# Optimization experiments

Measured on AMD Instinct MI355X. Metric: run time of the kernel, lower is better.

## Reference

```python
import jax, jax.numpy as jnp
import numpy as np

B, S, D = 2, 2048, 1024
H = 16
HD = D // H  # 64


def _rope_tables(seq_len, head_dim, dtype=jnp.float32):
    inv_freq = 1.0 / (10000.0 ** (jnp.arange(0, head_dim, 2, dtype=jnp.float32) / head_dim))
    t = jnp.arange(seq_len, dtype=jnp.float32)
    freqs = jnp.einsum('i,j->ij', t, inv_freq)            # [S, HD/2]
    emb = jnp.concatenate([freqs, freqs], axis=-1)        # [S, HD]
    return jnp.cos(emb).astype(dtype)[None, None], jnp.sin(emb).astype(dtype)[None, None]


def _rotate_half(x):
    x1, x2 = x[..., : x.shape[-1] // 2], x[..., x.shape[-1] // 2 :]
    return jnp.concatenate([-x2, x1], axis=-1)


def setup_inputs() -> dict:
    key = jax.random.key(0)
    ks = jax.random.split(key, 9)
    s = 0.02
    return {
        'hidden_states': jax.random.normal(ks[0], (B, S, D), jnp.float32),
        'attention_mask': jnp.zeros((B, 1, S, S), jnp.float32),
        'Wq': jax.random.normal(ks[1], (D, D), jnp.float32) * s,
        'bq': jnp.zeros((D,), jnp.float32),
        'Wk': jax.random.normal(ks[2], (D, D), jnp.float32) * s,
        'bk': jnp.zeros((D,), jnp.float32),
        'Wv': jax.random.normal(ks[3], (D, D), jnp.float32) * s,
        'bv': jnp.zeros((D,), jnp.float32),
        'Wo': jax.random.normal(ks[4], (D, D), jnp.float32) * s,
        'bo': jnp.zeros((D,), jnp.float32),
    }


def reference(hidden_states, attention_mask, Wq, bq, Wk, bk, Wv, bv, Wo, bo):
    b, s = hidden_states.shape[:2]
    q = hidden_states @ Wq.T + bq
    k = hidden_states @ Wk.T + bk
    v = hidden_states @ Wv.T + bv
    # [B, H, S, HD]
    q = q.reshape(b, s, H, HD).transpose(0, 2, 1, 3)
    k = k.reshape(b, s, H, HD).transpose(0, 2, 1, 3)
    v = v.reshape(b, s, H, HD).transpose(0, 2, 1, 3)
    cos, sin = _rope_tables(s, HD, q.dtype)
    q = q * cos + _rotate_half(q) * sin
    k = k * cos + _rotate_half(k) * sin
    scaling = HD ** (-0.5)
    scores = jnp.einsum('bhqd,bhkd->bhqk', q, k) * scaling
    scores = scores / jnp.log(jnp.asarray(float(s), scores.dtype))  # dynamic NTK
    scores = scores + attention_mask
    probs = jax.nn.softmax(scores, axis=-1)
    out = jnp.einsum('bhqk,bhkd->bhqd', probs, v)
    out = out.transpose(0, 2, 1, 3).reshape(b, s, H * HD)
    return out @ Wo.T + bo
```

## Files before the change

### kernel.cpp

```cpp
#include <hip/hip_runtime.h>
#include <math.h>

#define S_LEN 2048
#define NHEAD 16
#define HDIM  64

typedef __attribute__((ext_vector_type(8))) short bf16x8;
typedef __attribute__((ext_vector_type(4))) float f32x4;

__device__ __forceinline__ unsigned short f2bf(float f) {
    union { float f; unsigned u; } v; v.f = f;
    unsigned r = v.u + 0x7fffu + ((v.u >> 16) & 1u);
    return (unsigned short)(r >> 16);
}

__device__ __forceinline__ void gl2lds16(const void* g, void* l) {
    __builtin_amdgcn_global_load_lds(
        (__attribute__((address_space(1))) void*)(void*)(g),
        (__attribute__((address_space(3))) void*)(l), 16, 0, 0);
}

__global__ __launch_bounds__(256) void convert_kernel(
    const float* __restrict__ hs, const float* __restrict__ Wq,
    const float* __restrict__ Wk, const float* __restrict__ Wv,
    const float* __restrict__ Wo, unsigned short* __restrict__ dst,
    float2* __restrict__ rtab)
{
    const int bid = blockIdx.x;
    if (bid >= 8192) {
        const int gid = (bid - 8192) * 256 + threadIdx.x;
        const int s = gid >> 5, i = gid & 31;
        const float l2c = 0.41524101186092029f;
        const float freq = exp2f(-(float)i * l2c);
        const float ang = (float)s * freq;
        float2 cs;
        cs.x = cosf(ang);
        cs.y = sinf(ang);
        rtab[gid] = cs;
        return;
    }
    const int gid = bid * 256 + threadIdx.x;
    const int n = gid << 2;
    const float* src; int off;
    if (n < (4 << 20))      { src = hs; off = n; }
    else if (n < (5 << 20)) { src = Wq; off = n - (4 << 20); }
    else if (n < (6 << 20)) { src = Wk; off = n - (5 << 20); }
    else if (n < (7 << 20)) { src = Wv; off = n - (6 << 20); }
    else                    { src = Wo; off = n - (7 << 20); }
    const float4 v = *(const float4*)(src + off);
    ushort4 o;
    o.x = f2bf(v.x); o.y = f2bf(v.y); o.z = f2bf(v.z); o.w = f2bf(v.w);
    *(ushort4*)(dst + n) = o;
}

__global__ __launch_bounds__(256, 3) void qkv_gemm_kernel(
    const unsigned short* __restrict__ X,
    const unsigned short* __restrict__ Wall,
    const float* __restrict__ bq, const float* __restrict__ bk,
    const float* __restrict__ bv, const float2* __restrict__ rtab,
    unsigned short* __restrict__ qo, unsigned short* __restrict__ ko,
    unsigned short* __restrict__ vo)
{
    __shared__ unsigned short As[128 * 64];
    __shared__ unsigned short Bs[128 * 64];

    const int mat = blockIdx.x >> 3;
    const int n0  = (blockIdx.x & 7) << 7;
    const int m0  = blockIdx.y << 7;
    const unsigned short* W = Wall + (mat << 20);
    const float* bias = (mat == 0) ? bq : (mat == 1) ? bk : bv;
    unsigned short* out = (mat == 0) ? qo : (mat == 1) ? ko : vo;

    const int tid = threadIdx.x;
    const int wave = tid >> 6, lane = tid & 63;
    const int quad = lane >> 4, ln = lane & 15;
    const int wm = (wave >> 1) << 6, wn = (wave & 1) << 6;

    const unsigned short* xptr[4];
    const unsigned short* wptr[4];
    #pragma unroll
    for (int L = 0; L < 4; ++L) {
        const int i = tid + (L << 8);
        const int r = i >> 3, cl = i & 7;
        const int cg = (cl ^ (r & 7)) << 3;
        const int rq = r & 63;
        const int tau = (mat < 2)
            ? ((r & 64) | ((rq & 15) << 1) | ((rq >> 4) & 1) | (((rq >> 5) & 1) << 5))
            : ((r & 64) | ((rq & 15) << 2) | (rq >> 4));
        xptr[L] = X + (m0 + r) * 1024 + cg;
        wptr[L] = W + (n0 + tau) * 1024 + cg;
    }

    f32x4 acc[4][4] = {};

    for (int k0 = 0; k0 < 1024; k0 += 64) {
        #pragma unroll
        for (int L = 0; L < 4; ++L) {
            const int i = tid + (L << 8);
            gl2lds16(xptr[L] + k0, &As[i << 3]);
            gl2lds16(wptr[L] + k0, &Bs[i << 3]);
        }
        __syncthreads();
        #pragma unroll
        for (int s = 0; s < 2; ++s) {
            bf16x8 a[4], b[4];
            #pragma unroll
            for (int t = 0; t < 4; ++t) {
                const int ra = wm + (t << 4) + ln;
                a[t] = *(const bf16x8*)&As[(ra << 6) + ((((s << 2) | quad) ^ (ra & 7)) << 3)];
                const int rb = wn + (t << 4) + ln;
                b[t] = *(const bf16x8*)&Bs[(rb << 6) + ((((s << 2) | quad) ^ (rb & 7)) << 3)];
            }
            #pragma unroll
            for (int i = 0; i < 4; ++i)
                #pragma unroll
                for (int j = 0; j < 4; ++j)
                    acc[i][j] = __builtin_amdgcn_mfma_f32_16x16x32_bf16(a[i], b[j], acc[i][j], 0, 0, 0);
        }
        __syncthreads();
    }

    const int h = (n0 + wn) >> 6;

    if (mat < 2) {
        const int nb = n0 + wn + (ln << 1);
        const float b0 = bias[nb],      b1 = bias[nb + 1];
        const float b2 = bias[nb + 32], b3 = bias[nb + 33];
        #pragma unroll
        for (int i = 0; i < 4; ++i) {
            #pragma unroll
            for (int reg = 0; reg < 4; ++reg) {
                const int m = m0 + wm + (i << 4) + (quad << 2) + reg;
                const int b_ = m >> 11, s_ = m & 2047;
                unsigned short* o = out + ((((b_ << 4) + h) << 11) + s_) * 64;
                const float4 cs = *(const float4*)(rtab + (s_ << 5) + (ln << 1));
                const float x1a = acc[i][0][reg] + b0, x1b = acc[i][1][reg] + b1;
                const float x2a = acc[i][2][reg] + b2, x2b = acc[i][3][reg] + b3;
                const float r0a = x1a * cs.x - x2a * cs.y;
                const float r0b = x1b * cs.z - x2b * cs.w;
                const float r1a = x2a * cs.x + x1a * cs.y;
                const float r1b = x2b * cs.z + x1b * cs.w;
                const unsigned ua = __float_as_uint(r0a) + 0x8000u;
                const unsigned ub = __float_as_uint(r0b) + 0x8000u;
                const unsigned uc = __float_as_uint(r1a) + 0x8000u;
                const unsigned ud = __float_as_uint(r1b) + 0x8000u;
                *(unsigned*)(o + (ln << 1))      = __builtin_amdgcn_perm(ub, ua, 0x07060302u);
                *(unsigned*)(o + 32 + (ln << 1)) = __builtin_amdgcn_perm(ud, uc, 0x07060302u);
            }
        }
    } else {
        const float4 bv4 = *(const float4*)(bias + n0 + wn + (ln << 2));
        #pragma unroll
        for (int i = 0; i < 4; ++i)
            #pragma unroll
            for (int reg = 0; reg < 4; ++reg) {
                const int m = m0 + wm + (i << 4) + (quad << 2) + reg;
                const int b_ = m >> 11, s_ = m & 2047;
                unsigned short* o = out + ((((b_ << 4) + h) << 11) + s_) * 64;
                const unsigned ua = __float_as_uint(acc[i][0][reg] + bv4.x) + 0x8000u;
                const unsigned ub = __float_as_uint(acc[i][1][reg] + bv4.y) + 0x8000u;
                const unsigned uc = __float_as_uint(acc[i][2][reg] + bv4.z) + 0x8000u;
                const unsigned ud = __float_as_uint(acc[i][3][reg] + bv4.w) + 0x8000u;
                uint2 w;
                w.x = __builtin_amdgcn_perm(ub, ua, 0x07060302u);
                w.y = __builtin_amdgcn_perm(ud, uc, 0x07060302u);
                *(uint2*)(o + (ln << 2)) = w;
            }
    }
}

__global__ __launch_bounds__(256) void vtrans_kernel(
    const unsigned short* __restrict__ v, unsigned short* __restrict__ vt)
{
    __shared__ unsigned short T[64][66];
    const int bh = blockIdx.x >> 5;
    const int s0 = (blockIdx.x & 31) << 6;
    const int tid = threadIdx.x;
    #pragma unroll
    for (int L = 0; L < 4; ++L) {
        const int i = tid + (L << 8);
        const int r = i >> 4, c4 = (i & 15) << 2;
        const ushort4 in = *(const ushort4*)(v + ((bh << 11) + s0 + r) * 64 + c4);
        T[r][c4 + 0] = in.x; T[r][c4 + 1] = in.y;
        T[r][c4 + 2] = in.z; T[r][c4 + 3] = in.w;
    }
    __syncthreads();
    #pragma unroll
    for (int L = 0; L < 4; ++L) {
        const int i = tid + (L << 8);
        const int hd = i >> 4, c4 = (i & 15) << 2;
        ushort4 o;
        o.x = T[c4 + 0][hd]; o.y = T[c4 + 1][hd];
        o.z = T[c4 + 2][hd]; o.w = T[c4 + 3][hd];
        *(ushort4*)(vt + ((bh << 6) + hd) * 2048 + s0 + c4) = o;
    }
}

__global__ __launch_bounds__(512, 4) void flash_kernel(
    const unsigned short* __restrict__ qb, const unsigned short* __restrict__ kb,
    const unsigned short* __restrict__ vtb, const float* __restrict__ mask,
    unsigned short* __restrict__ attn)
{
    __shared__ unsigned short Ks[2][64 * 64];
    __shared__ unsigned short Vt[2][64 * 64];
    __shared__ unsigned short Ps[8 * 1024];

    const int qt = blockIdx.x & 15;
    const int bh = blockIdx.x >> 4;
    const int b_ = bh >> 4, h = bh & 15;
    const int q0 = qt << 7;

    const int tid = threadIdx.x;
    const int wave = tid >> 6, lane = tid & 63;
    const int quad = lane >> 4, ln = lane & 15;

    const unsigned short* qrow = qb + ((size_t)((bh << 11) + q0 + (wave << 4) + ln) << 6);
    bf16x8 qa0 = *(const bf16x8*)(qrow + (quad << 3));
    bf16x8 qa1 = *(const bf16x8*)(qrow + 32 + (quad << 3));

    const float scale = 0.125f / logf(2048.0f);

    unsigned short* Pw = Ps + (wave << 10);

    int kvo0[4], kvo1[4];
    #pragma unroll
    for (int j = 0; j < 4; ++j) {
        const int r = (j << 4) + ln;
        kvo0[j] = (r << 6) + ((quad ^ (r & 7)) << 3);
        kvo1[j] = kvo0[j] ^ 32;
    }
    int po[4];
    #pragma unroll
    for (int reg = 0; reg < 4; ++reg) {
        const int pr = (quad << 2) + reg;
        po[reg] = (pr << 6) + (((ln >> 1) ^ (pr & 7)) << 3) + ((ln & 1) << 2);
    }
    const int pro0 = (ln << 6) + ((quad ^ (ln & 7)) << 3);
    const int pro1 = pro0 ^ 32;

    const int r0 = tid >> 3, c0 = ((tid & 7) ^ (r0 & 7)) << 3;
    const int p0 = ((r0 & 15) << 2) + (r0 >> 4);
    const unsigned short* kg = kb + ((bh << 11) + p0) * 64 + c0;
    const unsigned short* vg = vtb + ((bh << 6) + r0) * 2048 + c0;
    const float* mptr = mask + ((size_t)b_ << 22)
                      + ((size_t)(q0 + (wave << 4) + (quad << 2)) << 11) + (ln << 2);

    float l_i[4] = {0.f, 0.f, 0.f, 0.f};
    f32x4 O[4] = {};

#define FLASH_SYNC()                                              \
    do {                                                          \
        asm volatile("s_waitcnt vmcnt(4)" ::: "memory");          \
        __builtin_amdgcn_s_barrier();                             \
    } while (0)
#define VMEM_PIN() asm volatile("" ::: "memory")

    gl2lds16(kg, &Ks[0][tid << 3]);
    gl2lds16(vg, &Vt[0][tid << 3]);
    VMEM_PIN();
    kg += 4096; vg += 64;
    float4 mA[4], mB[4];
    #pragma unroll
    for (int reg = 0; reg < 4; ++reg)
        mA[reg] = *(const float4*)(mptr + (reg << 11));
    mptr += 64;

#define FLASH_STEP(BUF, MR)                                                   \
    {                                                                         \
        f32x4 sacc[4] = {};                                                   \
        {                                                                     \
            bf16x8 bfr[4];                                                    \
            _Pragma("unroll")                                                 \
            for (int j = 0; j < 4; ++j)                                       \
                bfr[j] = *(const bf16x8*)&Ks[BUF][kvo0[j]];                   \
            __builtin_amdgcn_s_setprio(1);                                    \
            _Pragma("unroll")                                                 \
            for (int j = 0; j < 4; ++j)                                       \
                sacc[j] = __builtin_amdgcn_mfma_f32_16x16x32_bf16(            \
                    qa0, bfr[j], sacc[j], 0, 0, 0);                           \
            __builtin_amdgcn_s_setprio(0);                                    \
            _Pragma("unroll")                                                 \
            for (int j = 0; j < 4; ++j)                                       \
                bfr[j] = *(const bf16x8*)&Ks[BUF][kvo1[j]];                   \
            __builtin_amdgcn_s_setprio(1);                                    \
            _Pragma("unroll")                                                 \
            for (int j = 0; j < 4; ++j)                                       \
                sacc[j] = __builtin_amdgcn_mfma_f32_16x16x32_bf16(            \
                    qa1, bfr[j], sacc[j], 0, 0, 0);                           \
            __builtin_amdgcn_s_setprio(0);                                    \
        }                                                                     \
        _Pragma("unroll")                                                     \
        for (int reg = 0; reg < 4; ++reg) {                                   \
            float p0_ = __expf(fmaf(sacc[0][reg], scale, MR[reg].x));         \
            float p1_ = __expf(fmaf(sacc[1][reg], scale, MR[reg].y));         \
            float p2_ = __expf(fmaf(sacc[2][reg], scale, MR[reg].z));         \
            float p3_ = __expf(fmaf(sacc[3][reg], scale, MR[reg].w));         \
            l_i[reg] += (p0_ + p1_) + (p2_ + p3_);                            \
            unsigned u0 = __float_as_uint(p0_) + 0x8000u;                     \
            unsigned u1 = __float_as_uint(p1_) + 0x8000u;                     \
            unsigned u2 = __float_as_uint(p2_) + 0x8000u;                     \
            unsigned u3 = __float_as_uint(p3_) + 0x8000u;                     \
            uint2 w;                                                          \
            w.x = __builtin_amdgcn_perm(u1, u0, 0x07060302u);                 \
            w.y = __builtin_amdgcn_perm(u3, u2, 0x07060302u);                 \
            *(uint2*)&Pw[po[reg]] = w;                                        \
        }                                                                     \
        {                                                                     \
            bf16x8 a_ = *(const bf16x8*)&Pw[pro0];                            \
            bf16x8 bfr[4];                                                    \
            _Pragma("unroll")                                                 \
            for (int j = 0; j < 4; ++j)                                       \
                bfr[j] = *(const bf16x8*)&Vt[BUF][kvo0[j]];                   \
            __builtin_amdgcn_s_setprio(1);                                    \
            _Pragma("unroll")                                                 \
            for (int j = 0; j < 4; ++j)                                       \
                O[j] = __builtin_amdgcn_mfma_f32_16x16x32_bf16(               \
                    a_, bfr[j], O[j], 0, 0, 0);                               \
            __builtin_amdgcn_s_setprio(0);                                    \
            a_ = *(const bf16x8*)&Pw[pro1];                                   \
            _Pragma("unroll")                                                 \
            for (int j = 0; j < 4; ++j)                                       \
                bfr[j] = *(const bf16x8*)&Vt[BUF][kvo1[j]];                   \
            __builtin_amdgcn_s_setprio(1);                                    \
            _Pragma("unroll")                                                 \
            for (int j = 0; j < 4; ++j)                                       \
                O[j] = __builtin_amdgcn_mfma_f32_16x16x32_bf16(               \
                    a_, bfr[j], O[j], 0, 0, 0);                               \
            __builtin_amdgcn_s_setprio(0);                                    \
        }                                                                     \
    }

    for (int it = 0; it < 16; ++it) {
        FLASH_SYNC();
        gl2lds16(kg, &Ks[1][tid << 3]);
        gl2lds16(vg, &Vt[1][tid << 3]);
        VMEM_PIN();
        kg += 4096; vg += 64;
        #pragma unroll
        for (int reg = 0; reg < 4; ++reg)
            mB[reg] = *(const float4*)(mptr + (reg << 11));
        mptr += 64;

        FLASH_STEP(0, mA)

        FLASH_SYNC();
        if (it < 15) {
            gl2lds16(kg, &Ks[0][tid << 3]);
            gl2lds16(vg, &Vt[0][tid << 3]);
            VMEM_PIN();
            kg += 4096; vg += 64;
            #pragma unroll
            for (int reg = 0; reg < 4; ++reg)
                mA[reg] = *(const float4*)(mptr + (reg << 11));
            mptr += 64;
        }

        FLASH_STEP(1, mB)
    }
#undef FLASH_STEP
#undef FLASH_SYNC
#undef VMEM_PIN

    #pragma unroll
    for (int reg = 0; reg < 4; ++reg) {
        float l = l_i[reg];
        l += __shfl_xor(l, 1);
        l += __shfl_xor(l, 2);
        l += __shfl_xor(l, 4);
        l += __shfl_xor(l, 8);
        const float inv = 1.0f / l;
        const int qr = q0 + (wave << 4) + (quad << 2) + reg;
        unsigned short* op = attn + (((size_t)((b_ << 11) + qr)) << 10) + (h << 6);
        #pragma unroll
        for (int j = 0; j < 4; ++j)
            op[(j << 4) + ln] = f2bf(O[j][reg] * inv);
    }
}

__global__ __launch_bounds__(256, 3) void out_gemm_kernel(
    const unsigned short* __restrict__ X, const unsigned short* __restrict__ W,
    const float* __restrict__ bias, float* __restrict__ out)
{
    __shared__ unsigned short As[128 * 64];
    __shared__ unsigned short Bs[128 * 64];

    const int n0 = blockIdx.x << 7;
    const int m0 = blockIdx.y << 7;
    const int tid = threadIdx.x;
    const int wave = tid >> 6, lane = tid & 63;
    const int quad = lane >> 4, ln = lane & 15;
    const int wm = (wave >> 1) << 6, wn = (wave & 1) << 6;

    const unsigned short* xptr[4];
    const unsigned short* wptr[4];
    #pragma unroll
    for (int L = 0; L < 4; ++L) {
        const int i = tid + (L << 8);
        const int r = i >> 3, cl = i & 7;
        const int cg = (cl ^ (r & 7)) << 3;
        const int rq = r & 63;
        const int tau = (r & 64) | ((rq & 15) << 2) | (rq >> 4);
        xptr[L] = X + (m0 + r) * 1024 + cg;
        wptr[L] = W + (n0 + tau) * 1024 + cg;
    }

    f32x4 acc[4][4] = {};

    for (int k0 = 0; k0 < 1024; k0 += 64) {
        #pragma unroll
        for (int L = 0; L < 4; ++L) {
            const int i = tid + (L << 8);
            gl2lds16(xptr[L] + k0, &As[i << 3]);
            gl2lds16(wptr[L] + k0, &Bs[i << 3]);
        }
        __syncthreads();
        #pragma unroll
        for (int s = 0; s < 2; ++s) {
            bf16x8 a[4], b[4];
            #pragma unroll
            for (int t = 0; t < 4; ++t) {
                const int ra = wm + (t << 4) + ln;
                a[t] = *(const bf16x8*)&As[(ra << 6) + ((((s << 2) | quad) ^ (ra & 7)) << 3)];
                const int rb = wn + (t << 4) + ln;
                b[t] = *(const bf16x8*)&Bs[(rb << 6) + ((((s << 2) | quad) ^ (rb & 7)) << 3)];
            }
            #pragma unroll
            for (int i = 0; i < 4; ++i)
                #pragma unroll
                for (int j = 0; j < 4; ++j)
                    acc[i][j] = __builtin_amdgcn_mfma_f32_16x16x32_bf16(a[i], b[j], acc[i][j], 0, 0, 0);
        }
        __syncthreads();
    }

    const float4 bv4 = *(const float4*)(bias + n0 + wn + (ln << 2));

    #pragma unroll
    for (int i = 0; i < 4; ++i)
        #pragma unroll
        for (int reg = 0; reg < 4; ++reg) {
            const int m = m0 + wm + (i << 4) + (quad << 2) + reg;
            float4 ov;
            ov.x = acc[i][0][reg] + bv4.x;
            ov.y = acc[i][1][reg] + bv4.y;
            ov.z = acc[i][2][reg] + bv4.z;
            ov.w = acc[i][3][reg] + bv4.w;
            *(float4*)(out + m * 1024 + n0 + wn + (ln << 2)) = ov;
        }
}

extern "C" void kernel_launch(void* const* d_in, const int* in_sizes, int n_in,
                              void* d_out, int out_size, void* d_ws, size_t ws_size,
                              hipStream_t stream)
{
    const float* hs   = (const float*)d_in[0];
    const float* mask = (const float*)d_in[1];
    const float* Wq   = (const float*)d_in[2];
    const float* bq   = (const float*)d_in[3];
    const float* Wk   = (const float*)d_in[4];
    const float* bk   = (const float*)d_in[5];
    const float* Wv   = (const float*)d_in[6];
    const float* bv   = (const float*)d_in[7];
    const float* Wo   = (const float*)d_in[8];
    const float* bo   = (const float*)d_in[9];

    unsigned short* ws = (unsigned short*)d_ws;
    const size_t M1 = (size_t)1 << 20;
    unsigned short* hsb   = ws;
    unsigned short* wall  = ws + 4 * M1;
    unsigned short* wob   = ws + 7 * M1;
    unsigned short* qbf   = ws + 8 * M1;
    unsigned short* kbf   = ws + 12 * M1;
    unsigned short* vbf   = ws + 16 * M1;
    unsigned short* vtb   = ws + 20 * M1;
    unsigned short* attnb = ws + 24 * M1;
    float2*         rtab  = (float2*)(ws + 28 * M1);

    convert_kernel<<<8448, 256, 0, stream>>>(hs, Wq, Wk, Wv, Wo, ws, rtab);
    qkv_gemm_kernel<<<dim3(24, 32), 256, 0, stream>>>(hsb, wall, bq, bk, bv, rtab, qbf, kbf, vbf);
    vtrans_kernel<<<1024, 256, 0, stream>>>(vbf, vtb);
    flash_kernel<<<512, 512, 0, stream>>>(qbf, kbf, vtb, mask, attnb);
    out_gemm_kernel<<<dim3(8, 32), 256, 0, stream>>>(attnb, wob, bo, (float*)d_out);
}
```

Measured before the change: 226.6 us.

## Fuse V transpose into QKV GEMM epilogue and double-buffer output GEMM

The QKV GEMM epilogue for V now writes its bf16 results directly in transposed [B,H,HD,S] layout, so the separate vtrans kernel and its intermediate buffer are removed. The output projection GEMM gets double-buffered LDS staging, which overlaps the global-to-LDS loads of the next k-tile with the MFMA work on the current one. The V epilogue now issues strided 8-byte stores across rows of 2048, which may coalesce worse than before. Doubling LDS in the output GEMM lowers the occupancy hint from 3 to 2 blocks per CU.

```diff
diff --git a/kernel.cpp b/kernel.cpp
--- a/kernel.cpp
+++ b/kernel.cpp
@@ -150,49 +150,27 @@
         }
     } else {
         const float4 bv4 = *(const float4*)(bias + n0 + wn + (ln << 2));
-        #pragma unroll
-        for (int i = 0; i < 4; ++i)
-            #pragma unroll
-            for (int reg = 0; reg < 4; ++reg) {
-                const int m = m0 + wm + (i << 4) + (quad << 2) + reg;
-                const int b_ = m >> 11, s_ = m & 2047;
-                unsigned short* o = out + ((((b_ << 4) + h) << 11) + s_) * 64;
-                const unsigned ua = __float_as_uint(acc[i][0][reg] + bv4.x) + 0x8000u;
-                const unsigned ub = __float_as_uint(acc[i][1][reg] + bv4.y) + 0x8000u;
-                const unsigned uc = __float_as_uint(acc[i][2][reg] + bv4.z) + 0x8000u;
-                const unsigned ud = __float_as_uint(acc[i][3][reg] + bv4.w) + 0x8000u;
-                uint2 w;
-                w.x = __builtin_amdgcn_perm(ub, ua, 0x07060302u);
-                w.y = __builtin_amdgcn_perm(ud, uc, 0x07060302u);
-                *(uint2*)(o + (ln << 2)) = w;
-            }
-    }
-}
-
-__global__ __launch_bounds__(256) void vtrans_kernel(
-    const unsigned short* __restrict__ v, unsigned short* __restrict__ vt)
-{
-    __shared__ unsigned short T[64][66];
-    const int bh = blockIdx.x >> 5;
-    const int s0 = (blockIdx.x & 31) << 6;
-    const int tid = threadIdx.x;
-    #pragma unroll
-    for (int L = 0; L < 4; ++L) {
-        const int i = tid + (L << 8);
-        const int r = i >> 4, c4 = (i & 15) << 2;
-        const ushort4 in = *(const ushort4*)(v + ((bh << 11) + s0 + r) * 64 + c4);
-        T[r][c4 + 0] = in.x; T[r][c4 + 1] = in.y;
-        T[r][c4 + 2] = in.z; T[r][c4 + 3] = in.w;
-    }
-    __syncthreads();
-    #pragma unroll
-    for (int L = 0; L < 4; ++L) {
-        const int i = tid + (L << 8);
-        const int hd = i >> 4, c4 = (i & 15) << 2;
-        ushort4 o;
-        o.x = T[c4 + 0][hd]; o.y = T[c4 + 1][hd];
-        o.z = T[c4 + 2][hd]; o.w = T[c4 + 3][hd];
-        *(ushort4*)(vt + ((bh << 6) + hd) * 2048 + s0 + c4) = o;
+        const float bb0 = bv4.x, bb1 = bv4.y, bb2 = bv4.z, bb3 = bv4.w;
+        #pragma unroll
+        for (int i = 0; i < 4; ++i) {
+            const int m = m0 + wm + (i << 4) + (quad << 2);
+            const int b_ = m >> 11, s_ = m & 2047;
+            unsigned short* vt = out
+                + ((size_t)((((b_ << 4) + h) << 6) + (ln << 2)) * 2048) + s_;
+            ushort4 o4;
+            o4.x = f2bf(acc[i][0][0] + bb0); o4.y = f2bf(acc[i][0][1] + bb0);
+            o4.z = f2bf(acc[i][0][2] + bb0); o4.w = f2bf(acc[i][0][3] + bb0);
+            *(ushort4*)(vt) = o4;
+            o4.x = f2bf(acc[i][1][0] + bb1); o4.y = f2bf(acc[i][1][1] + bb1);
+            o4.z = f2bf(acc[i][1][2] + bb1); o4.w = f2bf(acc[i][1][3] + bb1);
+            *(ushort4*)(vt + 2048) = o4;
+            o4.x = f2bf(acc[i][2][0] + bb2); o4.y = f2bf(acc[i][2][1] + bb2);
+            o4.z = f2bf(acc[i][2][2] + bb2); o4.w = f2bf(acc[i][2][3] + bb2);
+            *(ushort4*)(vt + 4096) = o4;
+            o4.x = f2bf(acc[i][3][0] + bb3); o4.y = f2bf(acc[i][3][1] + bb3);
+            o4.z = f2bf(acc[i][3][2] + bb3); o4.w = f2bf(acc[i][3][3] + bb3);
+            *(ushort4*)(vt + 6144) = o4;
+        }
     }
 }
 
@@ -377,12 +355,12 @@
     }
 }
 
-__global__ __launch_bounds__(256, 3) void out_gemm_kernel(
+__global__ __launch_bounds__(256, 2) void out_gemm_kernel(
     const unsigned short* __restrict__ X, const unsigned short* __restrict__ W,
     const float* __restrict__ bias, float* __restrict__ out)
 {
-    __shared__ unsigned short As[128 * 64];
-    __shared__ unsigned short Bs[128 * 64];
+    __shared__ unsigned short As[2][128 * 64];
+    __shared__ unsigned short Bs[2][128 * 64];
 
     const int n0 = blockIdx.x << 7;
     const int m0 = blockIdx.y << 7;
@@ -406,32 +384,66 @@
 
     f32x4 acc[4][4] = {};
 
-    for (int k0 = 0; k0 < 1024; k0 += 64) {
-        #pragma unroll
-        for (int L = 0; L < 4; ++L) {
-            const int i = tid + (L << 8);
-            gl2lds16(xptr[L] + k0, &As[i << 3]);
-            gl2lds16(wptr[L] + k0, &Bs[i << 3]);
-        }
-        __syncthreads();
-        #pragma unroll
-        for (int s = 0; s < 2; ++s) {
-            bf16x8 a[4], b[4];
-            #pragma unroll
-            for (int t = 0; t < 4; ++t) {
-                const int ra = wm + (t << 4) + ln;
-                a[t] = *(const bf16x8*)&As[(ra << 6) + ((((s << 2) | quad) ^ (ra & 7)) << 3)];
-                const int rb = wn + (t << 4) + ln;
-                b[t] = *(const bf16x8*)&Bs[(rb << 6) + ((((s << 2) | quad) ^ (rb & 7)) << 3)];
-            }
-            #pragma unroll
-            for (int i = 0; i < 4; ++i)
-                #pragma unroll
-                for (int j = 0; j < 4; ++j)
-                    acc[i][j] = __builtin_amdgcn_mfma_f32_16x16x32_bf16(a[i], b[j], acc[i][j], 0, 0, 0);
-        }
-        __syncthreads();
-    }
+#define OG_STAGE(BUF, K0)                                                     \
+    {                                                                         \
+        _Pragma("unroll")                                                     \
+        for (int L = 0; L < 4; ++L) {                                         \
+            const int i = tid + (L << 8);                                     \
+            gl2lds16(xptr[L] + (K0), &As[BUF][i << 3]);                       \
+            gl2lds16(wptr[L] + (K0), &Bs[BUF][i << 3]);                       \
+        }                                                                     \
+    }
+
+#define OG_COMPUTE(BUF)                                                       \
+    {                                                                         \
+        _Pragma("unroll")                                                     \
+        for (int s = 0; s < 2; ++s) {                                         \
+            bf16x8 a[4], b[4];                                                \
+            _Pragma("unroll")                                                 \
+            for (int t_ = 0; t_ < 4; ++t_) {                                  \
+                const int ra = wm + (t_ << 4) + ln;                           \
+                a[t_] = *(const bf16x8*)&As[BUF][(ra << 6) +                  \
+                    ((((s << 2) | quad) ^ (ra & 7)) << 3)];                   \
+                const int rb = wn + (t_ << 4) + ln;                           \
+                b[t_] = *(const bf16x8*)&Bs[BUF][(rb << 6) +                  \
+                    ((((s << 2) | quad) ^ (rb & 7)) << 3)];                   \
+            }                                                                 \
+            _Pragma("unroll")                                                 \
+            for (int i = 0; i < 4; ++i)                                       \
+                _Pragma("unroll")                                             \
+                for (int j = 0; j < 4; ++j)                                   \
+                    acc[i][j] = __builtin_amdgcn_mfma_f32_16x16x32_bf16(      \
+                        a[i], b[j], acc[i][j], 0, 0, 0);                      \
+        }                                                                     \
+    }
+
+#define OG_SYNC()                                                 \
+    do {                                                          \
+        asm volatile("s_waitcnt vmcnt(0)" ::: "memory");          \
+        __builtin_amdgcn_s_barrier();                             \
+    } while (0)
+
+    OG_STAGE(0, 0)
+    OG_SYNC();
+
+    #pragma unroll 1
+    for (int t = 0; t < 7; ++t) {
+        const int k0 = t << 7;
+        OG_STAGE(1, k0 + 64)
+        OG_COMPUTE(0)
+        OG_SYNC();
+        OG_STAGE(0, k0 + 128)
+        OG_COMPUTE(1)
+        OG_SYNC();
+    }
+    OG_STAGE(1, 960)
+    OG_COMPUTE(0)
+    OG_SYNC();
+    OG_COMPUTE(1)
+
+#undef OG_SYNC
+#undef OG_COMPUTE
+#undef OG_STAGE
 
     const float4 bv4 = *(const float4*)(bias + n0 + wn + (ln << 2));
 
@@ -471,14 +483,12 @@
     unsigned short* wob   = ws + 7 * M1;
     unsigned short* qbf   = ws + 8 * M1;
     unsigned short* kbf   = ws + 12 * M1;
-    unsigned short* vbf   = ws + 16 * M1;
     unsigned short* vtb   = ws + 20 * M1;
     unsigned short* attnb = ws + 24 * M1;
     float2*         rtab  = (float2*)(ws + 28 * M1);
 
     convert_kernel<<<8448, 256, 0, stream>>>(hs, Wq, Wk, Wv, Wo, ws, rtab);
-    qkv_gemm_kernel<<<dim3(24, 32), 256, 0, stream>>>(hsb, wall, bq, bk, bv, rtab, qbf, kbf, vbf);
-    vtrans_kernel<<<1024, 256, 0, stream>>>(vbf, vtb);
-    flash_kernel<<<512, 512, 0, stream>>>(qbf, kbf, vtb, mask, attnb);
+    qkv_gemm_kernel<<<dim3(24, 32), 256, 0, stream>>>(hsb, wall, bq, bk, bv, rtab, qbf, kbf, vtb);
+    flash_kernel<<<1024 / 2, 512, 0, stream>>>(qbf, kbf, vtb, mask, attnb);
     out_gemm_kernel<<<dim3(8, 32), 256, 0, stream>>>(attnb, wob, bo, (float*)d_out);
 }
```

Result: no change. 228.9 us (+1.0%).
